# Kernel tuning notes

Measured on AMD Instinct MI355X. Metric: run time of the kernel, lower is better.

Reference implementation:

```python
import jax, jax.numpy as jnp
import numpy as np

D_MODEL = 512
NUM_HEADS = 8


def setup_inputs() -> dict:
    key = jax.random.key(0)
    ks = jax.random.split(key, 12)
    B, S, D = 2, 4096, D_MODEL
    s = 1.0 / np.sqrt(D)
    return {
        "q": jax.random.normal(ks[0], (B, S, D), jnp.float32),
        "k": jax.random.normal(ks[1], (B, S, D), jnp.float32),
        "v": jax.random.normal(ks[2], (B, S, D), jnp.float32),
        "w_q": jax.random.normal(ks[3], (D, D), jnp.float32) * s,
        "b_q": jax.random.normal(ks[4], (D,), jnp.float32) * s,
        "w_k": jax.random.normal(ks[5], (D, D), jnp.float32) * s,
        "b_k": jax.random.normal(ks[6], (D,), jnp.float32) * s,
        "w_v": jax.random.normal(ks[7], (D, D), jnp.float32) * s,
        "b_v": jax.random.normal(ks[8], (D,), jnp.float32) * s,
        "w_o": jax.random.normal(ks[9], (D, D), jnp.float32) * s,
        "b_o": jax.random.normal(ks[10], (D,), jnp.float32) * s,
    }


def _split(x, num_heads):
    B, S, D = x.shape
    return x.reshape(B, S, num_heads, D // num_heads).transpose(0, 2, 1, 3)


def reference(q, k, v, w_q, b_q, w_k, b_k, w_v, b_v, w_o, b_o):
    # Linear projections (torch Linear: x @ W^T + b)
    qp = q @ w_q.T + b_q
    kp = k @ w_k.T + b_k
    vp = v @ w_v.T + b_v
    # split into heads: [B, H, S, d_head]
    qh = _split(qp, NUM_HEADS)
    kh = _split(kp, NUM_HEADS)
    vh = _split(vp, NUM_HEADS)
    d_head = qh.shape[-1]
    # NOTE: original scales by sqrt(d_model of the per-head tensor) == sqrt(d_head)
    score = jnp.einsum("bhqd,bhkd->bhqk", qh, kh) / jnp.sqrt(jnp.float32(d_head))
    attn = jax.nn.softmax(score, axis=-1)  # full [B,H,S,S] materialized, as in source
    out = jnp.einsum("bhqk,bhkd->bhqd", attn, vh)
    # concat heads back to [B, S, D]
    B, H, S, Dh = out.shape
    out = out.transpose(0, 2, 1, 3).reshape(B, S, H * Dh)
    return out @ w_o.T + b_o
```

## Files before the change

### kernel.cpp

```cpp
#include <hip/hip_runtime.h>
#include <math.h>

typedef __bf16 bf16_t;
typedef __bf16 bf16x4_v __attribute__((ext_vector_type(4)));
typedef __bf16 bf16x8_t __attribute__((ext_vector_type(8)));
typedef float f32x4_t __attribute__((ext_vector_type(4)));
typedef unsigned uint2_t __attribute__((ext_vector_type(2)));
typedef unsigned uint4_t __attribute__((ext_vector_type(4)));

#define S_LEN 4096
#define DM 512
#define NH 8
#define DH 64
#define MTOT 8192

#define Q_SCALE 0.1803368801111204f

#define REG   4194304
#define WREG  262144
#define W_OFF (3 * REG)
#define CVT_TOTAL (3 * REG + 4 * WREG)
#define QH_OFF CVT_TOTAL

__device__ inline f32x4_t mfma16(bf16x8_t a, bf16x8_t b, f32x4_t c) {
    return __builtin_amdgcn_mfma_f32_16x16x32_bf16(a, b, c, 0, 0, 0);
}

__device__ inline unsigned pkbf16(float a, float b) {
    unsigned short ra = __builtin_bit_cast(unsigned short, (bf16_t)a);
    unsigned short rb = __builtin_bit_cast(unsigned short, (bf16_t)b);
    return (unsigned)ra | ((unsigned)rb << 16);
}

__device__ inline void async_copy16(const void* g, void* l) {
    __builtin_amdgcn_global_load_lds(
        (const __attribute__((address_space(1))) void*)g,
        (__attribute__((address_space(3))) void*)l, 16, 0, 0);
}

__global__ __launch_bounds__(256) void cvt_all(
    const float* __restrict__ q, const float* __restrict__ k, const float* __restrict__ v,
    const float* __restrict__ wq, const float* __restrict__ wk,
    const float* __restrict__ wv, const float* __restrict__ wo,
    bf16_t* __restrict__ dst)
{
    long gidx = (long)blockIdx.x * 2048 + (long)threadIdx.x * 8;
    const float* src;
    long off = gidx;
    if      (gidx < 1L * REG)          { src = q; }
    else if (gidx < 2L * REG)          { src = k;  off = gidx - 1L * REG; }
    else if (gidx < 3L * REG)          { src = v;  off = gidx - 2L * REG; }
    else if (gidx < W_OFF + 1L * WREG) { src = wq; off = gidx - W_OFF; }
    else if (gidx < W_OFF + 2L * WREG) { src = wk; off = gidx - (W_OFF + 1L * WREG); }
    else if (gidx < W_OFF + 3L * WREG) { src = wv; off = gidx - (W_OFF + 2L * WREG); }
    else                               { src = wo; off = gidx - (W_OFF + 3L * WREG); }
    float4 a = *(const float4*)(src + off);
    float4 b = *(const float4*)(src + off + 4);
    bf16x8_t h;
    h[0] = (bf16_t)a.x; h[1] = (bf16_t)a.y; h[2] = (bf16_t)a.z; h[3] = (bf16_t)a.w;
    h[4] = (bf16_t)b.x; h[5] = (bf16_t)b.y; h[6] = (bf16_t)b.z; h[7] = (bf16_t)b.w;
    *(bf16x8_t*)(dst + gidx) = h;
}

__global__ __launch_bounds__(256) void gemm_qkv(
    const bf16_t* __restrict__ XWb,
    const float* __restrict__ B0, const float* __restrict__ B1, const float* __restrict__ B2,
    bf16_t* __restrict__ dst_base)
{
    const int p = blockIdx.z;
    const bf16_t* __restrict__ X = XWb + (size_t)p * REG;
    const bf16_t* __restrict__ W = XWb + W_OFF + (size_t)p * WREG;
    const float* __restrict__ Bi = (p == 0) ? B0 : ((p == 1) ? B1 : B2);
    bf16_t* __restrict__ dst = dst_base + (size_t)p * REG;

    const int m0 = blockIdx.x * 128;
    const int n0 = blockIdx.y * 128;
    const int tid = threadIdx.x;
    const int lane = tid & 63, wid = tid >> 6;
    const int lm = lane & 15, lg = lane >> 4;
    const int wm = (wid >> 1) * 64, wn = (wid & 1) * 64;

    __shared__ __align__(16) bf16_t As[128 * 64];
    __shared__ __align__(16) bf16_t Bs[128 * 64];

    f32x4_t acc[4][4] = {};

    const int r0 = tid >> 3, c7 = tid & 7;
    const int cA0 = ((lg) ^ (lm & 7)) * 8;
    const int cA1 = ((4 + lg) ^ (lm & 7)) * 8;

    for (int kb = 0; kb < DM / 64; ++kb) {
        const int k0 = kb * 64;
#pragma unroll
        for (int i = 0; i < 4; ++i) {
            int row = i * 32 + r0;
            int ch = c7 ^ (row & 7);
            async_copy16(X + (size_t)(m0 + row) * DM + k0 + ch * 8, (char*)As + (i * 256 + tid) * 16);
            async_copy16(W + (size_t)(n0 + row) * DM + k0 + ch * 8, (char*)Bs + (i * 256 + tid) * 16);
        }
        __syncthreads();
#pragma unroll
        for (int kd = 0; kd < 2; ++kd) {
            const int co = kd ? cA1 : cA0;
            bf16x8_t fa[4], fb[4];
#pragma unroll
            for (int mt = 0; mt < 4; ++mt) {
                fa[mt] = *(const bf16x8_t*)(As + (wm + mt * 16 + lm) * 64 + co);
                fb[mt] = *(const bf16x8_t*)(Bs + (wn + mt * 16 + lm) * 64 + co);
            }
            if (p < 2) {
#pragma unroll
                for (int mt = 0; mt < 4; ++mt)
#pragma unroll
                    for (int nt = 0; nt < 4; ++nt)
                        acc[nt][mt] = mfma16(fb[nt], fa[mt], acc[nt][mt]);
            } else {
#pragma unroll
                for (int mt = 0; mt < 4; ++mt)
#pragma unroll
                    for (int nt = 0; nt < 4; ++nt)
                        acc[mt][nt] = mfma16(fa[mt], fb[nt], acc[mt][nt]);
            }
        }
        __syncthreads();
    }

    if (p == 2) {
#pragma unroll
        for (int nt = 0; nt < 4; ++nt) {
            int col = n0 + wn + nt * 16 + lm;
            float bv = Bi[col];
            int h = (col >> 6) & 7, dc = col & 63;
#pragma unroll
            for (int mt = 0; mt < 4; ++mt) {
                int mrow = m0 + wm + mt * 16 + lg * 4;
                int bb = mrow >> 12, s = mrow & (S_LEN - 1);
                bf16x4_v pk;
#pragma unroll
                for (int r = 0; r < 4; ++r) pk[r] = (bf16_t)(acc[mt][nt][r] + bv);
                *(bf16x4_v*)&dst[(((size_t)(bb * NH + h)) * DH + dc) * S_LEN + s] = pk;
            }
        }
    } else {
        const float scale = (p == 0) ? Q_SCALE : 1.0f;
#pragma unroll
        for (int nt = 0; nt < 4; ++nt) {
            int ncol = n0 + wn + nt * 16 + lg * 4;
            float4 bv4 = *(const float4*)&Bi[ncol];
            int h = (ncol >> 6) & 7, dc = ncol & 63;
#pragma unroll
            for (int mt = 0; mt < 4; ++mt) {
                int m = m0 + wm + mt * 16 + lm;
                int bb = m >> 12, s = m & (S_LEN - 1);
                bf16x4_v pk;
                pk[0] = (bf16_t)((acc[nt][mt][0] + bv4.x) * scale);
                pk[1] = (bf16_t)((acc[nt][mt][1] + bv4.y) * scale);
                pk[2] = (bf16_t)((acc[nt][mt][2] + bv4.z) * scale);
                pk[3] = (bf16_t)((acc[nt][mt][3] + bv4.w) * scale);
                *(bf16x4_v*)&dst[(((size_t)(bb * NH + h)) * S_LEN + s) * DH + dc] = pk;
            }
        }
    }
}

__global__ __launch_bounds__(512, 4) void flash_attn(
    const bf16_t* __restrict__ Qh, const bf16_t* __restrict__ Kh,
    const bf16_t* __restrict__ Vth, bf16_t* __restrict__ O)
{
    const int bh = blockIdx.y;
    const int q0 = blockIdx.x * 128;
    const int tid = threadIdx.x;
    const int lane = tid & 63, wid = tid >> 6;
    const int lm = lane & 15, lg = lane >> 4;
    const int qg = wid & 3;
    const int kvh = wid >> 2;

    const bf16_t* __restrict__ Qb  = Qh  + (size_t)bh * S_LEN * DH;
    const bf16_t* __restrict__ Kb  = Kh  + (size_t)bh * S_LEN * DH;
    const bf16_t* __restrict__ Vtg = Vth + (size_t)bh * S_LEN * DH;

    __shared__ __align__(16) char smem[65536];

    bf16x8_t bQ[2][2];
#pragma unroll
    for (int nt = 0; nt < 2; ++nt)
#pragma unroll
        for (int kd = 0; kd < 2; ++kd)
            bQ[nt][kd] = *(const bf16x8_t*)(Qb + (size_t)(q0 + qg * 32 + nt * 16 + lm) * DH + kd * 32 + lg * 8);

    f32x4_t o_acc[4][2] = {};
    float l_acc[2] = {0.f, 0.f};

    const int srow = tid >> 3;
    const int slch = (tid & 7) ^ (srow & 7);
    const bf16_t* gK = Kb + (size_t)srow * DH + slch * 8;
    const bf16_t* gV = Vtg + (size_t)srow * S_LEN + slch * 8;

    const int cK0 = ((lg) ^ (lm & 7)) * 16;
    const int cK1 = ((4 + lg) ^ (lm & 7)) * 16;

    {
        char* b = smem;
        async_copy16(gK, b + tid * 16);
        async_copy16(gK + (size_t)64 * DH, b + 8192 + tid * 16);
        async_copy16(gV, b + 16384 + tid * 16);
        async_copy16(gV + 64, b + 24576 + tid * 16);
    }

    const int NT = S_LEN / 128;
    for (int it = 0; it < NT; ++it) {
        const char* buf = smem + (it & 1) * 32768;
        __syncthreads();

        if (it + 1 < NT) {
            char* nb = smem + ((it + 1) & 1) * 32768;
            const int kvb = (it + 1) * 128;
            async_copy16(gK + (size_t)kvb * DH, nb + tid * 16);
            async_copy16(gK + (size_t)(kvb + 64) * DH, nb + 8192 + tid * 16);
            async_copy16(gV + kvb, nb + 16384 + tid * 16);
            async_copy16(gV + kvb + 64, nb + 24576 + tid * 16);
        }

        const char* ksb = buf + kvh * 8192;
        const char* vsb = buf + 16384 + kvh * 8192;

        unsigned pk[4][2][2];
#pragma unroll
        for (int mt = 0; mt < 4; ++mt) {
            const char* krow = ksb + (mt * 16 + lm) * 128;
            bf16x8_t aK0 = *(const bf16x8_t*)(krow + cK0);
            bf16x8_t aK1 = *(const bf16x8_t*)(krow + cK1);
            f32x4_t s0 = {}, s1 = {};
            s0 = mfma16(aK0, bQ[0][0], s0);
            s0 = mfma16(aK1, bQ[0][1], s0);
            s1 = mfma16(aK0, bQ[1][0], s1);
            s1 = mfma16(aK1, bQ[1][1], s1);
            float e0 = __builtin_amdgcn_exp2f(s0[0]);
            float e1 = __builtin_amdgcn_exp2f(s0[1]);
            float e2 = __builtin_amdgcn_exp2f(s0[2]);
            float e3 = __builtin_amdgcn_exp2f(s0[3]);
            pk[mt][0][0] = pkbf16(e0, e1);
            pk[mt][0][1] = pkbf16(e2, e3);
            l_acc[0] += (e0 + e1) + (e2 + e3);
            float f0 = __builtin_amdgcn_exp2f(s1[0]);
            float f1 = __builtin_amdgcn_exp2f(s1[1]);
            float f2 = __builtin_amdgcn_exp2f(s1[2]);
            float f3 = __builtin_amdgcn_exp2f(s1[3]);
            pk[mt][1][0] = pkbf16(f0, f1);
            pk[mt][1][1] = pkbf16(f2, f3);
            l_acc[1] += (f0 + f1) + (f2 + f3);
        }

#pragma unroll
        for (int mt = 0; mt < 4; ++mt) {
            const char* vrow = vsb + (mt * 16 + lm) * 128;
#pragma unroll
            for (int cc = 0; cc < 2; ++cc) {
                const int ca = 2 * cc, cb = 2 * cc + 1;
                int pc0 = (ca * 2 + (lg >> 1)) ^ (lm & 7);
                int pc1 = (cb * 2 + (lg >> 1)) ^ (lm & 7);
                uint2_t va0 = *(const uint2_t*)(vrow + pc0 * 16 + (lg & 1) * 8);
                uint2_t va1 = *(const uint2_t*)(vrow + pc1 * 16 + (lg & 1) * 8);
                bf16x8_t vA = __builtin_bit_cast(bf16x8_t, (uint4_t){va0[0], va0[1], va1[0], va1[1]});
                bf16x8_t bP0 = __builtin_bit_cast(bf16x8_t, (uint4_t){pk[ca][0][0], pk[ca][0][1], pk[cb][0][0], pk[cb][0][1]});
                bf16x8_t bP1 = __builtin_bit_cast(bf16x8_t, (uint4_t){pk[ca][1][0], pk[ca][1][1], pk[cb][1][0], pk[cb][1][1]});
                o_acc[mt][0] = mfma16(vA, bP0, o_acc[mt][0]);
                o_acc[mt][1] = mfma16(vA, bP1, o_acc[mt][1]);
            }
        }
    }

#pragma unroll
    for (int nt = 0; nt < 2; ++nt) {
        l_acc[nt] += __shfl_xor(l_acc[nt], 16, 64);
        l_acc[nt] += __shfl_xor(l_acc[nt], 32, 64);
    }

    __syncthreads();

    float* ob = (float*)smem + qg * (32 * 66);
    float* lb = (float*)(smem + 33792);

    if (kvh == 1) {
#pragma unroll
        for (int nt = 0; nt < 2; ++nt) {
#pragma unroll
            for (int mt = 0; mt < 4; ++mt)
#pragma unroll
                for (int r = 0; r < 4; ++r)
                    ob[(nt * 16 + lm) * 66 + mt * 16 + lg * 4 + r] = o_acc[mt][nt][r];
            if (lg == 0) lb[qg * 32 + nt * 16 + lm] = l_acc[nt];
        }
    }
    __syncthreads();
    if (kvh == 0) {
        const int bb = bh >> 3, h = bh & 7;
#pragma unroll
        for (int nt = 0; nt < 2; ++nt) {
            float ltot = l_acc[nt] + lb[qg * 32 + nt * 16 + lm];
            float inv = 1.0f / ltot;
            int q = q0 + qg * 32 + nt * 16 + lm;
            size_t base = ((size_t)(bb * S_LEN + q)) * DM + h * DH;
#pragma unroll
            for (int mt = 0; mt < 4; ++mt) {
                const float* orow = &ob[(nt * 16 + lm) * 66 + mt * 16 + lg * 4];
                bf16x4_v pkd;
#pragma unroll
                for (int r = 0; r < 4; ++r)
                    pkd[r] = (bf16_t)((o_acc[mt][nt][r] + orow[r]) * inv);
                *(bf16x4_v*)&O[base + mt * 16 + lg * 4] = pkd;
            }
        }
    }
}

__global__ __launch_bounds__(256) void gemm_out(
    const bf16_t* __restrict__ A, const bf16_t* __restrict__ W,
    const float* __restrict__ Bi, float* __restrict__ out)
{
    const int m0 = blockIdx.x * 64;
    const int n0 = blockIdx.y * 128;
    const int tid = threadIdx.x;
    const int lane = tid & 63, wid = tid >> 6;
    const int lm = lane & 15, lg = lane >> 4;
    const int wm = (wid >> 1) * 32, wn = (wid & 1) * 64;

    __shared__ __align__(16) bf16_t As[64 * 64];
    __shared__ __align__(16) bf16_t Bs[128 * 64];

    f32x4_t acc[4][2] = {};

    const int r0 = tid >> 3, c7 = tid & 7;
    const int cA0 = ((lg) ^ (lm & 7)) * 8;
    const int cA1 = ((4 + lg) ^ (lm & 7)) * 8;

    for (int kb = 0; kb < DM / 64; ++kb) {
        const int k0 = kb * 64;
#pragma unroll
        for (int i = 0; i < 2; ++i) {
            int idx = i * 256 + tid;
            int row = idx >> 3;
            int ch = (idx & 7) ^ (row & 7);
            async_copy16(A + (size_t)(m0 + row) * DM + k0 + ch * 8, (char*)As + idx * 16);
        }
#pragma unroll
        for (int i = 0; i < 4; ++i) {
            int row = i * 32 + r0;
            int ch = c7 ^ (row & 7);
            async_copy16(W + (size_t)(n0 + row) * DM + k0 + ch * 8, (char*)Bs + (i * 256 + tid) * 16);
        }
        __syncthreads();
#pragma unroll
        for (int kd = 0; kd < 2; ++kd) {
            const int co = kd ? cA1 : cA0;
            bf16x8_t fa[2], fb[4];
#pragma unroll
            for (int mt = 0; mt < 2; ++mt)
                fa[mt] = *(const bf16x8_t*)(As + (wm + mt * 16 + lm) * 64 + co);
#pragma unroll
            for (int nt = 0; nt < 4; ++nt)
                fb[nt] = *(const bf16x8_t*)(Bs + (wn + nt * 16 + lm) * 64 + co);
#pragma unroll
            for (int nt = 0; nt < 4; ++nt)
#pragma unroll
                for (int mt = 0; mt < 2; ++mt)
                    acc[nt][mt] = mfma16(fb[nt], fa[mt], acc[nt][mt]);
        }
        __syncthreads();
    }

#pragma unroll
    for (int nt = 0; nt < 4; ++nt) {
        int ncol = n0 + wn + nt * 16 + lg * 4;
        float4 bv4 = *(const float4*)&Bi[ncol];
#pragma unroll
        for (int mt = 0; mt < 2; ++mt) {
            int m = m0 + wm + mt * 16 + lm;
            float4 ov;
            ov.x = acc[nt][mt][0] + bv4.x;
            ov.y = acc[nt][mt][1] + bv4.y;
            ov.z = acc[nt][mt][2] + bv4.z;
            ov.w = acc[nt][mt][3] + bv4.w;
            *(float4*)&out[(size_t)m * DM + ncol] = ov;
        }
    }
}

extern "C" void kernel_launch(void* const* d_in, const int* in_sizes, int n_in,
                              void* d_out, int out_size, void* d_ws, size_t ws_size,
                              hipStream_t stream)
{
    const float* q  = (const float*)d_in[0];
    const float* k  = (const float*)d_in[1];
    const float* v  = (const float*)d_in[2];
    const float* wq = (const float*)d_in[3];
    const float* bq = (const float*)d_in[4];
    const float* wk = (const float*)d_in[5];
    const float* bk = (const float*)d_in[6];
    const float* wv = (const float*)d_in[7];
    const float* bv = (const float*)d_in[8];
    const float* wo = (const float*)d_in[9];
    const float* bo = (const float*)d_in[10];
    float* out = (float*)d_out;

    bf16_t* ws = (bf16_t*)d_ws;
    bf16_t* XWb = ws;
    bf16_t* Qh  = ws + QH_OFF;
    bf16_t* Kh  = Qh + REG;
    bf16_t* VTh = Kh + REG;
    bf16_t* Ob  = ws;
    bf16_t* Wob = ws + W_OFF + 3 * (size_t)WREG;

    cvt_all<<<CVT_TOTAL / 2048, 256, 0, stream>>>(q, k, v, wq, wk, wv, wo, XWb);

    dim3 g1(MTOT / 128, DM / 128, 3);
    gemm_qkv<<<g1, 256, 0, stream>>>(XWb, bq, bk, bv, Qh);

    dim3 g2(S_LEN / 128, 2 * NH, 1);
    flash_attn<<<g2, 512, 0, stream>>>(Qh, Kh, VTh, Ob);

    dim3 g3(MTOT / 64, DM / 128, 1);
    gemm_out<<<g3, 256, 0, stream>>>(Ob, Wob, bo, out);
}
```

Before: 226.2 us.

## Halve flash-attention block to 4 waves, each handling 64 query rows

The attention kernel now runs 4 waves instead of 8 per 128-query block. Each wave owns 64 query rows instead of 32, so every K and V fragment read from LDS feeds twice as many MFMAs, which cuts LDS traffic per FLOP. Each thread now issues twice as many async loads per tile, and the cross-wave reduction writes full float4 vectors with a padded stride of 68. The price is higher register pressure (double the O accumulators and P registers), lower occupancy from the launch bound of (256,2), and fewer waves per block to hide latency.

```diff
diff --git a/kernel.cpp b/kernel.cpp
--- a/kernel.cpp
+++ b/kernel.cpp
@@ -163,7 +163,7 @@
     }
 }
 
-__global__ __launch_bounds__(512, 4) void flash_attn(
+__global__ __launch_bounds__(256, 2) void flash_attn(
     const bf16_t* __restrict__ Qh, const bf16_t* __restrict__ Kh,
     const bf16_t* __restrict__ Vth, bf16_t* __restrict__ O)
 {
@@ -172,8 +172,8 @@
     const int tid = threadIdx.x;
     const int lane = tid & 63, wid = tid >> 6;
     const int lm = lane & 15, lg = lane >> 4;
-    const int qg = wid & 3;
-    const int kvh = wid >> 2;
+    const int qg = wid & 1;
+    const int kvh = wid >> 1;
 
     const bf16_t* __restrict__ Qb  = Qh  + (size_t)bh * S_LEN * DH;
     const bf16_t* __restrict__ Kb  = Kh  + (size_t)bh * S_LEN * DH;
@@ -181,15 +181,15 @@
 
     __shared__ __align__(16) char smem[65536];
 
-    bf16x8_t bQ[2][2];
-#pragma unroll
-    for (int nt = 0; nt < 2; ++nt)
+    bf16x8_t bQ[4][2];
+#pragma unroll
+    for (int nt = 0; nt < 4; ++nt)
 #pragma unroll
         for (int kd = 0; kd < 2; ++kd)
-            bQ[nt][kd] = *(const bf16x8_t*)(Qb + (size_t)(q0 + qg * 32 + nt * 16 + lm) * DH + kd * 32 + lg * 8);
-
-    f32x4_t o_acc[4][2] = {};
-    float l_acc[2] = {0.f, 0.f};
+            bQ[nt][kd] = *(const bf16x8_t*)(Qb + (size_t)(q0 + qg * 64 + nt * 16 + lm) * DH + kd * 32 + lg * 8);
+
+    f32x4_t o_acc[4][4] = {};
+    float l_acc[4] = {0.f, 0.f, 0.f, 0.f};
 
     const int srow = tid >> 3;
     const int slch = (tid & 7) ^ (srow & 7);
@@ -201,10 +201,13 @@
 
     {
         char* b = smem;
-        async_copy16(gK, b + tid * 16);
-        async_copy16(gK + (size_t)64 * DH, b + 8192 + tid * 16);
-        async_copy16(gV, b + 16384 + tid * 16);
-        async_copy16(gV + 64, b + 24576 + tid * 16);
+#pragma unroll
+        for (int i = 0; i < 4; ++i)
+            async_copy16(gK + (size_t)(32 * i) * DH, b + i * 4096 + tid * 16);
+#pragma unroll
+        for (int i = 0; i < 4; ++i)
+            async_copy16(gV + (size_t)(i & 1) * 32 * S_LEN + (i >> 1) * 64,
+                         b + 16384 + i * 4096 + tid * 16);
     }
 
     const int NT = S_LEN / 128;
@@ -215,40 +218,37 @@
         if (it + 1 < NT) {
             char* nb = smem + ((it + 1) & 1) * 32768;
             const int kvb = (it + 1) * 128;
-            async_copy16(gK + (size_t)kvb * DH, nb + tid * 16);
-            async_copy16(gK + (size_t)(kvb + 64) * DH, nb + 8192 + tid * 16);
-            async_copy16(gV + kvb, nb + 16384 + tid * 16);
-            async_copy16(gV + kvb + 64, nb + 24576 + tid * 16);
+#pragma unroll
+            for (int i = 0; i < 4; ++i)
+                async_copy16(gK + (size_t)(kvb + 32 * i) * DH, nb + i * 4096 + tid * 16);
+#pragma unroll
+            for (int i = 0; i < 4; ++i)
+                async_copy16(gV + (size_t)(i & 1) * 32 * S_LEN + kvb + (i >> 1) * 64,
+                             nb + 16384 + i * 4096 + tid * 16);
         }
 
         const char* ksb = buf + kvh * 8192;
         const char* vsb = buf + 16384 + kvh * 8192;
 
-        unsigned pk[4][2][2];
+        unsigned pk[4][4][2];
 #pragma unroll
         for (int mt = 0; mt < 4; ++mt) {
             const char* krow = ksb + (mt * 16 + lm) * 128;
             bf16x8_t aK0 = *(const bf16x8_t*)(krow + cK0);
             bf16x8_t aK1 = *(const bf16x8_t*)(krow + cK1);
-            f32x4_t s0 = {}, s1 = {};
-            s0 = mfma16(aK0, bQ[0][0], s0);
-            s0 = mfma16(aK1, bQ[0][1], s0);
-            s1 = mfma16(aK0, bQ[1][0], s1);
-            s1 = mfma16(aK1, bQ[1][1], s1);
-            float e0 = __builtin_amdgcn_exp2f(s0[0]);
-            float e1 = __builtin_amdgcn_exp2f(s0[1]);
-            float e2 = __builtin_amdgcn_exp2f(s0[2]);
-            float e3 = __builtin_amdgcn_exp2f(s0[3]);
-            pk[mt][0][0] = pkbf16(e0, e1);
-            pk[mt][0][1] = pkbf16(e2, e3);
-            l_acc[0] += (e0 + e1) + (e2 + e3);
-            float f0 = __builtin_amdgcn_exp2f(s1[0]);
-            float f1 = __builtin_amdgcn_exp2f(s1[1]);
-            float f2 = __builtin_amdgcn_exp2f(s1[2]);
-            float f3 = __builtin_amdgcn_exp2f(s1[3]);
-            pk[mt][1][0] = pkbf16(f0, f1);
-            pk[mt][1][1] = pkbf16(f2, f3);
-            l_acc[1] += (f0 + f1) + (f2 + f3);
+#pragma unroll
+            for (int nt = 0; nt < 4; ++nt) {
+                f32x4_t s = {};
+                s = mfma16(aK0, bQ[nt][0], s);
+                s = mfma16(aK1, bQ[nt][1], s);
+                float e0 = __builtin_amdgcn_exp2f(s[0]);
+                float e1 = __builtin_amdgcn_exp2f(s[1]);
+                float e2 = __builtin_amdgcn_exp2f(s[2]);
+                float e3 = __builtin_amdgcn_exp2f(s[3]);
+                pk[mt][nt][0] = pkbf16(e0, e1);
+                pk[mt][nt][1] = pkbf16(e2, e3);
+                l_acc[nt] += (e0 + e1) + (e2 + e3);
+            }
         }
 
 #pragma unroll
@@ -262,48 +262,48 @@
                 uint2_t va0 = *(const uint2_t*)(vrow + pc0 * 16 + (lg & 1) * 8);
                 uint2_t va1 = *(const uint2_t*)(vrow + pc1 * 16 + (lg & 1) * 8);
                 bf16x8_t vA = __builtin_bit_cast(bf16x8_t, (uint4_t){va0[0], va0[1], va1[0], va1[1]});
-                bf16x8_t bP0 = __builtin_bit_cast(bf16x8_t, (uint4_t){pk[ca][0][0], pk[ca][0][1], pk[cb][0][0], pk[cb][0][1]});
-                bf16x8_t bP1 = __builtin_bit_cast(bf16x8_t, (uint4_t){pk[ca][1][0], pk[ca][1][1], pk[cb][1][0], pk[cb][1][1]});
-                o_acc[mt][0] = mfma16(vA, bP0, o_acc[mt][0]);
-                o_acc[mt][1] = mfma16(vA, bP1, o_acc[mt][1]);
-            }
-        }
-    }
-
-#pragma unroll
-    for (int nt = 0; nt < 2; ++nt) {
+#pragma unroll
+                for (int nt = 0; nt < 4; ++nt) {
+                    bf16x8_t bP = __builtin_bit_cast(bf16x8_t,
+                        (uint4_t){pk[ca][nt][0], pk[ca][nt][1], pk[cb][nt][0], pk[cb][nt][1]});
+                    o_acc[mt][nt] = mfma16(vA, bP, o_acc[mt][nt]);
+                }
+            }
+        }
+    }
+
+#pragma unroll
+    for (int nt = 0; nt < 4; ++nt) {
         l_acc[nt] += __shfl_xor(l_acc[nt], 16, 64);
         l_acc[nt] += __shfl_xor(l_acc[nt], 32, 64);
     }
 
     __syncthreads();
 
-    float* ob = (float*)smem + qg * (32 * 66);
-    float* lb = (float*)(smem + 33792);
+    float* ob = (float*)smem + qg * (64 * 68);
+    float* lb = (float*)(smem + 34816);
 
     if (kvh == 1) {
 #pragma unroll
-        for (int nt = 0; nt < 2; ++nt) {
+        for (int nt = 0; nt < 4; ++nt) {
 #pragma unroll
             for (int mt = 0; mt < 4; ++mt)
-#pragma unroll
-                for (int r = 0; r < 4; ++r)
-                    ob[(nt * 16 + lm) * 66 + mt * 16 + lg * 4 + r] = o_acc[mt][nt][r];
-            if (lg == 0) lb[qg * 32 + nt * 16 + lm] = l_acc[nt];
+                *(f32x4_t*)&ob[(nt * 16 + lm) * 68 + mt * 16 + lg * 4] = o_acc[mt][nt];
+            if (lg == 0) lb[qg * 64 + nt * 16 + lm] = l_acc[nt];
         }
     }
     __syncthreads();
     if (kvh == 0) {
         const int bb = bh >> 3, h = bh & 7;
 #pragma unroll
-        for (int nt = 0; nt < 2; ++nt) {
-            float ltot = l_acc[nt] + lb[qg * 32 + nt * 16 + lm];
+        for (int nt = 0; nt < 4; ++nt) {
+            float ltot = l_acc[nt] + lb[qg * 64 + nt * 16 + lm];
             float inv = 1.0f / ltot;
-            int q = q0 + qg * 32 + nt * 16 + lm;
+            int q = q0 + qg * 64 + nt * 16 + lm;
             size_t base = ((size_t)(bb * S_LEN + q)) * DM + h * DH;
 #pragma unroll
             for (int mt = 0; mt < 4; ++mt) {
-                const float* orow = &ob[(nt * 16 + lm) * 66 + mt * 16 + lg * 4];
+                f32x4_t orow = *(const f32x4_t*)&ob[(nt * 16 + lm) * 68 + mt * 16 + lg * 4];
                 bf16x4_v pkd;
 #pragma unroll
                 for (int r = 0; r < 4; ++r)
@@ -417,7 +417,7 @@
     gemm_qkv<<<g1, 256, 0, stream>>>(XWb, bq, bk, bv, Qh);
 
     dim3 g2(S_LEN / 128, 2 * NH, 1);
-    flash_attn<<<g2, 512, 0, stream>>>(Qh, Kh, VTh, Ob);
+    flash_attn<<<g2, 256, 0, stream>>>(Qh, Kh, VTh, Ob);
 
     dim3 g3(MTOT / 64, DM / 128, 1);
     gemm_out<<<g3, 256, 0, stream>>>(Ob, Wob, bo, out);
```

Result: faster. 220.2 us (-2.7%).
